# Optimization experiments

Hardware: AMD Instinct MI355X
Metric: run time of the kernel (lower is better)

Reference implementation:

```python
import jax, jax.numpy as jnp
import numpy as np

B, C, H, W = 2, 256, 128, 128
L, NH, NP = 4, 8, 4
D = C // NH
HW = H * W


def _pos_emb_2d(h, w, c):
    # positional_encodings.PositionalEncoding2D for channels-last input (B, h, w, c)
    ch = int(np.ceil(c / 4) * 2)
    inv_freq = 1.0 / (10000.0 ** (np.arange(0, ch, 2, dtype=np.float32) / ch))

    def emb(n):
        s = np.arange(n, dtype=np.float32)[:, None] * inv_freq[None, :]
        return np.stack([np.sin(s), np.cos(s)], -1).reshape(n, -1)  # interleaved sin/cos

    out = np.zeros((h, w, 2 * ch), np.float32)
    out[:, :, :ch] = emb(h)[:, None, :]
    out[:, :, ch:2 * ch] = emb(w)[None, :, :]
    return jnp.asarray(out[:, :, :c])


def _offset_bias():
    # init_weights grid_init bias of sampling_offsets
    thetas = np.arange(NH, dtype=np.float32) * (2.0 * np.pi / NH)
    g = np.stack([np.cos(thetas), np.sin(thetas)], -1)
    g = g / np.abs(g).max(-1, keepdims=True)
    g = np.tile(g[:, None, None, :], (1, 1, NP, 1))
    for i in range(NP):
        g[:, :, i, :] *= i + 1
    return np.tile(g.reshape(-1)[None], (L, 1)).astype(np.float32)


def _ref_points(h, w):
    # get_reference_points with scale_ratio == 1 (ratio of equal lidar ranges)
    ry, rx = jnp.meshgrid(jnp.linspace(0.5, h - 0.5, h) / h,
                          jnp.linspace(0.5, w - 0.5, w) / w, indexing='ij')
    return jnp.stack([rx.reshape(-1), ry.reshape(-1)], -1)  # (HW, 2) as (x, y)


def _deform_attn(value, loc, aw, h, w):
    # value: (B,HW,NH,D); loc in [0,1]: (B,HW,NH,NP,2); aw: (B,HW,NH,NP)
    # Matches F.grid_sample(mode='bilinear', padding_mode='zeros', align_corners=False)
    b, q, nh, d = value.shape
    p = loc.shape[3]
    v = value.transpose(0, 2, 1, 3)  # (B, NH, HW, D)
    gx = 2.0 * loc[..., 0] - 1.0
    gy = 2.0 * loc[..., 1] - 1.0
    ix = ((gx + 1.0) * w - 1.0) * 0.5
    iy = ((gy + 1.0) * h - 1.0) * 0.5
    x0 = jnp.floor(ix)
    y0 = jnp.floor(iy)

    def gather(xf, yf):
        valid = (xf >= 0) & (xf <= w - 1) & (yf >= 0) & (yf <= h - 1)
        xi = jnp.clip(xf, 0, w - 1).astype(jnp.int32)
        yi = jnp.clip(yf, 0, h - 1).astype(jnp.int32)
        idx = (yi * w + xi).transpose(0, 2, 1, 3).reshape(b, nh, q * p)
        g = jnp.take_along_axis(v, idx[..., None], axis=2).reshape(b, nh, q, p, d)
        return g * valid.transpose(0, 2, 1, 3)[..., None]

    wx1 = (ix - x0).transpose(0, 2, 1, 3)[..., None]
    wy1 = (iy - y0).transpose(0, 2, 1, 3)[..., None]
    wx0 = 1.0 - wx1
    wy0 = 1.0 - wy1
    s = (gather(x0, y0) * (wx0 * wy0) + gather(x0 + 1.0, y0) * (wx1 * wy0)
         + gather(x0, y0 + 1.0) * (wx0 * wy1) + gather(x0 + 1.0, y0 + 1.0) * (wx1 * wy1))
    out = jnp.einsum('bhqpd,bqhp->bqhd', s, aw)
    return out.reshape(b, q, nh * d)


def setup_inputs() -> dict:
    key = jax.random.key(0)
    ks = jax.random.split(key, 8)
    sc = 1.0 / np.sqrt(C).astype(np.float32)
    return {
        "ego_feature": jax.random.normal(ks[0], (B, C, H, W), jnp.float32),
        "conv_w": jax.random.normal(ks[1], (C, C), jnp.float32) * sc,  # 1x1 conv, (in,out)
        "conv_b": jnp.zeros((C,), jnp.float32),
        "in_scale": jnp.ones((1,), jnp.float32) / 30.0,
        "out_scale": jnp.ones((1,), jnp.float32) / 30.0,
        "off_w": jax.random.normal(ks[2], (L, C, NH * NP * 2), jnp.float32) * 0.01,
        "off_b": jnp.asarray(_offset_bias()),
        "aw_w": jax.random.normal(ks[3], (L, C, NH * NP), jnp.float32) * 0.02,
        "aw_b": jnp.zeros((L, NH * NP), jnp.float32),
        "vp_w": jax.random.normal(ks[4], (L, C, C), jnp.float32) * sc,
        "vp_b": jnp.zeros((L, C), jnp.float32),
        "op_w": jax.random.normal(ks[5], (L, C, C), jnp.float32) * sc,
        "op_b": jnp.zeros((L, C), jnp.float32),
    }


def reference(ego_feature, conv_w, conv_b, in_scale, out_scale, off_w, off_b,
              aw_w, aw_b, vp_w, vp_b, op_w, op_b):
    # PositionalEncodingPermute2D: channels-last PE, permuted to (C,H,W)
    pe_in = _pos_emb_2d(H, W, C).transpose(2, 0, 1)[None]  # (1,C,H,W)
    x = ego_feature + in_scale[0] * pe_in
    key_tok = x.reshape(B, C, HW).transpose(0, 2, 1)  # (B, HW, C)
    # Upsample(scale=1) is identity; 1x1 conv == per-token matmul
    out = key_tok @ conv_w + conv_b
    pe_out = _pos_emb_2d(H, W, C)[None]  # (1,H,W,C)
    ref = _ref_points(H, W)
    norm = jnp.asarray([W, H], jnp.float32)
    for l in range(L):
        o = out.reshape(B, H, W, C) + out_scale[0] * pe_out
        q = o.reshape(B, HW, C)
        identity = q
        v = (key_tok @ vp_w[l] + vp_b[l]).reshape(B, HW, NH, D)
        offs = (q @ off_w[l] + off_b[l]).reshape(B, HW, NH, NP, 2)
        aw = jax.nn.softmax((q @ aw_w[l] + aw_b[l]).reshape(B, HW, NH, NP), axis=-1)
        loc = ref[None, :, None, None, :] + offs / norm
        attn = _deform_attn(v, loc, aw, H, W)
        out = attn @ op_w[l] + op_b[l] + identity  # dropout is identity in eval
    return out  # (B, HW, C)
```

## Files before the change

kernel.cpp:

```cpp
#include <hip/hip_runtime.h>
#include <math.h>

#define HH 128
#define WW 128
#define CCH 256
#define NHH 8
#define NPP 4
#define DDIM 32
#define HWW (HH * WW)
#define BB 2
#define MM (BB * HWW)
#define KK 256

typedef __attribute__((ext_vector_type(8))) __bf16 bf16x8;
typedef __attribute__((ext_vector_type(8))) short s16x8;
typedef __attribute__((ext_vector_type(4))) short s16x4;
typedef __attribute__((ext_vector_type(4))) float f32x4;

#define PE_LOG2_STEP 0.20762050593f

__device__ __forceinline__ float pe_val(int c, int y, int x) {
    int j = (c & 127) >> 1;
    float pos = (c < 128) ? (float)y : (float)x;
    float f = exp2f(-(float)j * PE_LOG2_STEP);
    float s, cs;
    __sincosf(pos * f, &s, &cs);
    return (c & 1) ? cs : s;
}

__device__ __forceinline__ short f2b(float f) {
    union { float f; unsigned u; } c; c.f = f;
    unsigned r = c.u + 0x7FFF + ((c.u >> 16) & 1);
    return (short)(r >> 16);
}

__device__ __forceinline__ float b2f(short s) {
    union { unsigned u; float f; } c;
    c.u = ((unsigned)(unsigned short)s) << 16;
    return c.f;
}

__device__ __forceinline__ void gload16(const short* g, short* l) {
    __builtin_amdgcn_global_load_lds(
        (const __attribute__((address_space(1))) unsigned int*)g,
        (__attribute__((address_space(3))) unsigned int*)l, 16, 0, 0);
}

__global__ __launch_bounds__(256) void pe_table_kernel(
    const float* __restrict__ out_scale, short* __restrict__ pe_b)
{
    int t = blockIdx.x * 256 + threadIdx.x;
    int cp = t & 127;
    int p = t >> 7;
    int y = p >> 7, x = p & 127;
    int c2 = cp * 2;
    int j = (c2 & 127) >> 1;
    float pos = (c2 < 128) ? (float)y : (float)x;
    float f = exp2f(-(float)j * PE_LOG2_STEP);
    float s, c;
    __sincosf(pos * f, &s, &c);
    float sc = out_scale[0];
    pe_b[(size_t)p * CCH + c2] = f2b(sc * s);
    pe_b[(size_t)p * CCH + c2 + 1] = f2b(sc * c);
}

__global__ __launch_bounds__(256) void convert_big_w(
    const float* __restrict__ conv_w, const float* __restrict__ vp_w,
    const float* __restrict__ op_w, short* __restrict__ wt)
{
    __shared__ float tile[32][33];
    int z = blockIdx.z;
    const float* src = (z == 0) ? conv_w
                     : (z <= 4) ? vp_w + (size_t)(z - 1) * KK * CCH
                                : op_w + (size_t)(z - 5) * KK * CCH;
    short* dst = wt + (size_t)z * KK * CCH;
    int k0 = blockIdx.x * 32, n0 = blockIdx.y * 32;
    int tx = threadIdx.x, ty = threadIdx.y;
    #pragma unroll
    for (int i = 0; i < 4; ++i)
        tile[ty + i * 8][tx] = src[(size_t)(k0 + ty + i * 8) * CCH + n0 + tx];
    __syncthreads();
    int t = ty * 32 + tx;
    int n_l = t >> 3, ks = (t & 7) * 4;
    s16x4 o;
    #pragma unroll
    for (int j = 0; j < 4; ++j) o[j] = f2b(tile[ks + j][n_l]);
    *(s16x4*)&dst[(size_t)(n0 + n_l) * KK + k0 + ks] = o;
}

__global__ __launch_bounds__(256) void convert_offaw_w(
    const float* __restrict__ off_w, const float* __restrict__ aw_w,
    const float* __restrict__ off_b, const float* __restrict__ aw_b,
    short* __restrict__ wt, float* __restrict__ bias_cat)
{
    __shared__ float tile[32][33];
    int l = blockIdx.z;
    int nt = blockIdx.y;
    int k0 = blockIdx.x * 32;
    const float* src; int N, ncol0;
    if (nt < 2) { src = off_w + (size_t)l * KK * 64; N = 64; ncol0 = nt * 32; }
    else        { src = aw_w + (size_t)l * KK * 32; N = 32; ncol0 = 0; }
    int tx = threadIdx.x, ty = threadIdx.y;
    #pragma unroll
    for (int i = 0; i < 4; ++i)
        tile[ty + i * 8][tx] = src[(size_t)(k0 + ty + i * 8) * N + ncol0 + tx];
    __syncthreads();
    int t = ty * 32 + tx;
    int n_l = t >> 3, ks = (t & 7) * 4;
    s16x4 o;
    #pragma unroll
    for (int j = 0; j < 4; ++j) o[j] = f2b(tile[ks + j][n_l]);
    *(s16x4*)&wt[((size_t)l * 96 + nt * 32 + n_l) * KK + k0 + ks] = o;
    if (blockIdx.x == 0 && t < 32) {
        int col = nt * 32 + t;
        bias_cat[l * 96 + col] = (nt < 2) ? off_b[l * 64 + ncol0 + t]
                                          : aw_b[l * 32 + t];
    }
}

__global__ __launch_bounds__(256) void transpose_pe_kernel(
    const float* __restrict__ ego, const float* __restrict__ in_scale,
    short* __restrict__ ktb)
{
    __shared__ float tile[32][33];
    int b = blockIdx.z;
    int c0 = blockIdx.x * 32;
    int p0 = blockIdx.y * 32;
    int tx = threadIdx.x, ty = threadIdx.y;
    const float* egob = ego + (size_t)b * CCH * HWW;
    #pragma unroll
    for (int i = 0; i < 4; ++i)
        tile[ty + i * 8][tx] = egob[(size_t)(c0 + ty + i * 8) * HWW + p0 + tx];
    __syncthreads();
    float isc = in_scale[0];
    int t = ty * 32 + tx;
    int p_l = t >> 3, cs = (t & 7) * 4;
    int p = p0 + p_l;
    int y = p >> 7, x = p & 127;
    s16x4 o;
    #pragma unroll
    for (int j = 0; j < 4; ++j) {
        int c = c0 + cs + j;
        o[j] = f2b(tile[cs + j][p_l] + isc * pe_val(c, y, x));
    }
    *(s16x4*)&ktb[((size_t)b * HWW + p) * CCH + c0 + cs] = o;
}

__device__ __forceinline__ void stage_slab64(
    const short* __restrict__ src, short* As, int m0, int w, int lane)
{
    #pragma unroll
    for (int i = 0; i < 8; ++i) {
        int c = w * 64 + i * 256;
        int cc = c + lane;
        int r = cc >> 5, col = cc & 31, ks = col >> 3, u = col & 7;
        gload16(src + (size_t)(m0 + r) * KK + ks * 64 + ((u ^ (r & 7)) << 3),
                As + c * 8);
    }
}

template<int NINST>
__device__ __forceinline__ void stage_tile(
    const short* __restrict__ src, short* dst, int row0, int ks, int w, int lane)
{
    #pragma unroll
    for (int i = 0; i < NINST; ++i) {
        int c = w * 64 + i * 256;
        int cc = c + lane;
        int r = cc >> 3, u = cc & 7;
        gload16(src + (size_t)(row0 + r) * KK + ks * 64 + ((u ^ (r & 7)) << 3),
                dst + c * 8);
    }
}

template<int BM, int BN, int WM, int WN>
__device__ __forceinline__ void gemm_core_db(
    const short* __restrict__ A, const short* __restrict__ Bt,
    short* AsBase, short* BsBase, int m0, int n0, int tid,
    f32x4 (&acc)[WM / 16][WN / 16])
{
    constexpr int MF = WM / 16, NF = WN / 16;
    constexpr int WAVES_N = BN / WN;
    constexpr int A_INST = (BM * 8) / 256;
    constexpr int B_INST = (BN * 8) / 256;
    int w = tid >> 6, lane = tid & 63;
    int g = lane >> 4, l16 = lane & 15;
    int wr = w / WAVES_N, wc = w % WAVES_N;
    short* As0 = AsBase; short* As1 = AsBase + BM * 64;
    short* Bs0 = BsBase; short* Bs1 = BsBase + BN * 64;

    stage_tile<A_INST>(A, As0, m0, 0, w, lane);
    stage_tile<B_INST>(Bt, Bs0, n0, 0, w, lane);
    asm volatile("s_waitcnt vmcnt(0)" ::: "memory");
    __syncthreads();

    #pragma unroll
    for (int ks = 0; ks < 4; ++ks) {
        short* Ac = (ks & 1) ? As1 : As0;
        short* Bc = (ks & 1) ? Bs1 : Bs0;
        short* An = (ks & 1) ? As0 : As1;
        short* Bn = (ks & 1) ? Bs0 : Bs1;
        if (ks < 3) {
            stage_tile<A_INST>(A, An, m0, ks + 1, w, lane);
            stage_tile<B_INST>(Bt, Bn, n0, ks + 1, w, lane);
        }
        #pragma unroll
        for (int kh = 0; kh < 2; ++kh) {
            bf16x8 af[MF], bfr[NF];
            #pragma unroll
            for (int mf = 0; mf < MF; ++mf) {
                int r = wr * WM + mf * 16 + l16, s = kh * 4 + g;
                af[mf] = *(const bf16x8*)(Ac + r * 64 + ((s ^ (r & 7)) * 8));
            }
            #pragma unroll
            for (int nf = 0; nf < NF; ++nf) {
                int r = wc * WN + nf * 16 + l16, s = kh * 4 + g;
                bfr[nf] = *(const bf16x8*)(Bc + r * 64 + ((s ^ (r & 7)) * 8));
            }
            #pragma unroll
            for (int mf = 0; mf < MF; ++mf)
                #pragma unroll
                for (int nf = 0; nf < NF; ++nf)
                    acc[mf][nf] = __builtin_amdgcn_mfma_f32_16x16x32_bf16(
                        af[mf], bfr[nf], acc[mf][nf], 0, 0, 0);
        }
        if (ks < 3) {
            __builtin_amdgcn_sched_barrier(0);
            asm volatile("s_waitcnt vmcnt(0)" ::: "memory");
            __syncthreads();
        }
    }
}

__global__ __launch_bounds__(256) void gemm_conv_v(
    const short* __restrict__ ktb, const short* __restrict__ wt_big,
    const float* __restrict__ conv_b, const float* __restrict__ vp_b,
    const short* __restrict__ pe_b, short* __restrict__ qb,
    short* __restrict__ vb16)
{
    __shared__ short As[64 * 256];
    __shared__ short Bs[128 * 64];
    int tid = threadIdx.x;
    int w = tid >> 6, lane = tid & 63;
    int g = lane >> 4, l16 = lane & 15;
    int wr = w >> 1, wc = w & 1;
    int flat = blockIdx.x;
    int xcd = flat & 7;
    int idx = flat >> 3;
    int mloc = idx & 63;
    int n0 = (idx >> 6) * 128;
    int m0 = (xcd * 64 + mloc) * 64;

    stage_slab64(ktb, As, m0, w, lane);
    s16x8 rb[4];
    #pragma unroll
    for (int i = 0; i < 4; ++i) {
        int task = tid + i * 256; int r = task >> 3, s = task & 7;
        rb[i] = *(const s16x8*)(wt_big + (size_t)(n0 + r) * KK + s * 8);
    }
    asm volatile("s_waitcnt vmcnt(0)" ::: "memory");
    __syncthreads();

    bf16x8 afr[4][2][2];
    #pragma unroll
    for (int ks = 0; ks < 4; ++ks)
        #pragma unroll
        for (int kh = 0; kh < 2; ++kh)
            #pragma unroll
            for (int mf = 0; mf < 2; ++mf) {
                int s = kh * 4 + g;
                int r = wr * 32 + mf * 16 + l16;
                afr[ks][kh][mf] =
                    *(const bf16x8*)(As + r * 256 + (ks * 8 + (s ^ (r & 7))) * 8);
            }

    for (int z = 0; z < 5; ++z) {
        f32x4 acc[2][4] = {};
        #pragma unroll
        for (int ks = 0; ks < 4; ++ks) {
            __syncthreads();
            #pragma unroll
            for (int i = 0; i < 4; ++i) {
                int task = tid + i * 256; int r = task >> 3, s = task & 7;
                *(s16x8*)&Bs[r * 64 + ((s ^ (r & 7)) * 8)] = rb[i];
            }
            __syncthreads();
            if (ks < 3) {
                const short* Bz = wt_big + (size_t)z * KK * CCH;
                #pragma unroll
                for (int i = 0; i < 4; ++i) {
                    int task = tid + i * 256; int r = task >> 3, s = task & 7;
                    rb[i] = *(const s16x8*)(Bz + (size_t)(n0 + r) * KK + (ks + 1) * 64 + s * 8);
                }
            } else if (z < 4) {
                const short* Bz = wt_big + (size_t)(z + 1) * KK * CCH;
                #pragma unroll
                for (int i = 0; i < 4; ++i) {
                    int task = tid + i * 256; int r = task >> 3, s = task & 7;
                    rb[i] = *(const s16x8*)(Bz + (size_t)(n0 + r) * KK + s * 8);
                }
            }
            #pragma unroll
            for (int kh = 0; kh < 2; ++kh) {
                int s = kh * 4 + g;
                bf16x8 bfr[4];
                #pragma unroll
                for (int nf = 0; nf < 4; ++nf) {
                    int r = wc * 64 + nf * 16 + l16;
                    bfr[nf] = *(const bf16x8*)(Bs + r * 64 + ((s ^ (r & 7)) * 8));
                }
                #pragma unroll
                for (int mf = 0; mf < 2; ++mf)
                    #pragma unroll
                    for (int nf = 0; nf < 4; ++nf)
                        acc[mf][nf] = __builtin_amdgcn_mfma_f32_16x16x32_bf16(
                            afr[ks][kh][mf], bfr[nf], acc[mf][nf], 0, 0, 0);
            }
        }
        const float* bias = (z == 0) ? conv_b : vp_b + (size_t)(z - 1) * CCH;
        short* vz = vb16 + (size_t)(z - 1) * MM * CCH;
        #pragma unroll
        for (int mf = 0; mf < 2; ++mf) {
            #pragma unroll
            for (int nf = 0; nf < 4; ++nf) {
                int col = n0 + wc * 64 + nf * 16 + l16;
                float bv = bias[col];
                #pragma unroll
                for (int j = 0; j < 4; ++j) {
                    int row = m0 + wr * 32 + mf * 16 + g * 4 + j;
                    float vv = acc[mf][nf][j] + bv;
                    if (z == 0) {
                        int p = row & (HWW - 1);
                        qb[(size_t)row * CCH + col] =
                            f2b(vv + b2f(pe_b[(size_t)p * CCH + col]));
                    } else {
                        int b = row >> 14, p = row & (HWW - 1);
                        int h = col >> 5, d = col & 31;
                        vz[(((size_t)(b * NHH + h)) * HWW + p) * DDIM + d] = f2b(vv);
                    }
                }
            }
        }
    }
}

__global__ __launch_bounds__(256) void gemm_scores(
    const short* __restrict__ qb, const short* __restrict__ wt,
    const float* __restrict__ bias, float* __restrict__ scores)
{
    __shared__ short As[2 * 64 * 64];
    __shared__ short Bs[2 * 96 * 64];
    int tid = threadIdx.x;
    int m0 = blockIdx.y * 64;
    f32x4 acc[2][3] = {};
    gemm_core_db<64, 96, 32, 48>(qb, wt, As, Bs, m0, 0, tid, acc);

    int w = tid >> 6, lane = tid & 63;
    int g = lane >> 4, l16 = lane & 15;
    int wr = w >> 1, wc = w & 1;
    #pragma unroll
    for (int mf = 0; mf < 2; ++mf) {
        #pragma unroll
        for (int nf = 0; nf < 3; ++nf) {
            int col = wc * 48 + nf * 16 + l16;
            float bv = bias[col];
            #pragma unroll
            for (int j = 0; j < 4; ++j) {
                int row = m0 + wr * 32 + mf * 16 + g * 4 + j;
                scores[(size_t)row * 96 + col] = acc[mf][nf][j] + bv;
            }
        }
    }
}

template<bool FINAL>
__global__ __launch_bounds__(256) void gemm_op(
    const short* __restrict__ attnb, const short* __restrict__ wt,
    const float* __restrict__ bias, const short* __restrict__ pe_b,
    float* __restrict__ outf, short* __restrict__ qb)
{
    __shared__ short As[2 * 128 * 64];
    __shared__ short Bs[2 * 128 * 64];
    int tid = threadIdx.x;
    int flat = blockIdx.x;
    int xcd = flat & 7;
    int idx = flat >> 3;
    int mloc = idx & 31;
    int n0 = (idx >> 5) * 128;
    int m0 = (xcd * 32 + mloc) * 128;
    f32x4 acc[4][4] = {};
    gemm_core_db<128, 128, 64, 64>(attnb, wt, As, Bs, m0, n0, tid, acc);

    int w = tid >> 6, lane = tid & 63;
    int g = lane >> 4, l16 = lane & 15;
    int wr = w >> 1, wc = w & 1;
    #pragma unroll
    for (int mf = 0; mf < 4; ++mf) {
        #pragma unroll
        for (int nf = 0; nf < 4; ++nf) {
            int col = n0 + wc * 64 + nf * 16 + l16;
            float bv = bias[col];
            #pragma unroll
            for (int j = 0; j < 4; ++j) {
                int row = m0 + wr * 64 + mf * 16 + g * 4 + j;
                float vv = acc[mf][nf][j] + bv + b2f(qb[(size_t)row * CCH + col]);
                if (FINAL) {
                    outf[(size_t)row * CCH + col] = vv;
                } else {
                    int p = row & (HWW - 1);
                    qb[(size_t)row * CCH + col] =
                        f2b(vv + b2f(pe_b[(size_t)p * CCH + col]));
                }
            }
        }
    }
}

__device__ __forceinline__ void fma8(uint4 u, float w, float* a) {
    a[0] = fmaf(__uint_as_float(u.x << 16), w, a[0]);
    a[1] = fmaf(__uint_as_float(u.x & 0xffff0000u), w, a[1]);
    a[2] = fmaf(__uint_as_float(u.y << 16), w, a[2]);
    a[3] = fmaf(__uint_as_float(u.y & 0xffff0000u), w, a[3]);
    a[4] = fmaf(__uint_as_float(u.z << 16), w, a[4]);
    a[5] = fmaf(__uint_as_float(u.z & 0xffff0000u), w, a[5]);
    a[6] = fmaf(__uint_as_float(u.w << 16), w, a[6]);
    a[7] = fmaf(__uint_as_float(u.w & 0xffff0000u), w, a[7]);
}

__global__ __launch_bounds__(256) void deform_kernel(
    const short* __restrict__ vb16, const float* __restrict__ scores,
    short* __restrict__ attnb)
{
    int tid = threadIdx.x;
    int gi = tid >> 2;
    int dl = (tid & 3) * 8;
    long gid = (long)blockIdx.x * 64 + gi;
    int h = (int)(gid & 7);
    long bp = gid >> 3;
    int p = (int)(bp & (HWW - 1));
    int b = (int)(bp >> 14);
    int y = p >> 7, x = p & 127;
    const float* srow = scores + bp * 96;
    float4 sc4 = *(const float4*)(srow + 64 + h * 4);
    float mx = fmaxf(fmaxf(sc4.x, sc4.y), fmaxf(sc4.z, sc4.w));
    float e0 = __expf(sc4.x - mx), e1 = __expf(sc4.y - mx);
    float e2 = __expf(sc4.z - mx), e3 = __expf(sc4.w - mx);
    float inv = 1.f / (e0 + e1 + e2 + e3);
    float wa4[4] = {e0 * inv, e1 * inv, e2 * inv, e3 * inv};
    float4 o01 = *(const float4*)(srow + h * 8);
    float4 o23 = *(const float4*)(srow + h * 8 + 4);
    float oxs[4] = {o01.x, o01.z, o23.x, o23.z};
    float oys[4] = {o01.y, o01.w, o23.y, o23.w};
    const short* vbase = vb16 + ((size_t)(b * NHH + h) * HWW) * DDIM + dl;
    float a[8] = {};
    #pragma unroll
    for (int pt = 0; pt < NPP; ++pt) {
        float wa = wa4[pt];
        float ix = (float)x + oxs[pt];
        float iy = (float)y + oys[pt];
        float x0f = floorf(ix), y0f = floorf(iy);
        float fx = ix - x0f, fy = iy - y0f;
        float wx0 = (x0f >= 0.f && x0f <= 127.f) ? (1.f - fx) : 0.f;
        float wx1 = (x0f >= -1.f && x0f <= 126.f) ? fx : 0.f;
        float wy0 = ((y0f >= 0.f && y0f <= 127.f) ? (1.f - fy) : 0.f) * wa;
        float wy1 = ((y0f >= -1.f && y0f <= 126.f) ? fy : 0.f) * wa;
        int xi0 = (int)fminf(fmaxf(x0f, 0.f), 127.f);
        int yi0 = (int)fminf(fmaxf(y0f, 0.f), 127.f);
        int xi1 = (int)fminf(fmaxf(x0f + 1.f, 0.f), 127.f);
        int yi1 = (int)fminf(fmaxf(y0f + 1.f, 0.f), 127.f);
        int r0 = yi0 << 7, r1 = yi1 << 7;
        uint4 u00 = *(const uint4*)(vbase + (size_t)(r0 + xi0) * DDIM);
        uint4 u01 = *(const uint4*)(vbase + (size_t)(r0 + xi1) * DDIM);
        uint4 u10 = *(const uint4*)(vbase + (size_t)(r1 + xi0) * DDIM);
        uint4 u11 = *(const uint4*)(vbase + (size_t)(r1 + xi1) * DDIM);
        fma8(u00, wx0 * wy0, a);
        fma8(u01, wx1 * wy0, a);
        fma8(u10, wx0 * wy1, a);
        fma8(u11, wx1 * wy1, a);
    }
    s16x8 o;
    #pragma unroll
    for (int j = 0; j < 8; ++j) o[j] = f2b(a[j]);
    *(s16x8*)&attnb[bp * CCH + h * DDIM + dl] = o;
}

extern "C" void kernel_launch(void* const* d_in, const int* in_sizes, int n_in,
                              void* d_out, int out_size, void* d_ws, size_t ws_size,
                              hipStream_t stream) {
    const float* ego       = (const float*)d_in[0];
    const float* conv_w    = (const float*)d_in[1];
    const float* conv_b    = (const float*)d_in[2];
    const float* in_scale  = (const float*)d_in[3];
    const float* out_scale = (const float*)d_in[4];
    const float* off_w     = (const float*)d_in[5];
    const float* off_b     = (const float*)d_in[6];
    const float* aw_w      = (const float*)d_in[7];
    const float* aw_b      = (const float*)d_in[8];
    const float* vp_w      = (const float*)d_in[9];
    const float* vp_b      = (const float*)d_in[10];
    const float* op_w      = (const float*)d_in[11];
    const float* op_b      = (const float*)d_in[12];
    float* out = (float*)d_out;

    float* scores   = (float*)d_ws;
    float* bias_cat = scores + (size_t)MM * 96;
    short* pe_b     = (short*)(bias_cat + 4 * 96);
    short* ktb      = pe_b + (size_t)HWW * CCH;
    short* qb       = ktb + (size_t)MM * CCH;
    short* vb16     = qb + (size_t)MM * CCH;
    short* attnb    = vb16 + (size_t)4 * MM * CCH;
    short* wt_big   = attnb + (size_t)MM * CCH;
    short* wt_offaw = wt_big + (size_t)9 * KK * CCH;

    pe_table_kernel<<<HWW * 128 / 256, 256, 0, stream>>>(out_scale, pe_b);
    convert_big_w<<<dim3(8, 8, 9), dim3(32, 8), 0, stream>>>(conv_w, vp_w, op_w, wt_big);
    convert_offaw_w<<<dim3(8, 3, 4), dim3(32, 8), 0, stream>>>(
        off_w, aw_w, off_b, aw_b, wt_offaw, bias_cat);
    transpose_pe_kernel<<<dim3(8, 512, 2), dim3(32, 8), 0, stream>>>(ego, in_scale, ktb);

    gemm_conv_v<<<1024, 256, 0, stream>>>(
        ktb, wt_big, conv_b, vp_b, pe_b, qb, vb16);

    for (int l = 0; l < 4; ++l) {
        gemm_scores<<<dim3(1, 512), 256, 0, stream>>>(
            qb, wt_offaw + (size_t)l * 96 * KK, bias_cat + l * 96, scores);
        deform_kernel<<<MM * NHH / 64, 256, 0, stream>>>(
            vb16 + (size_t)l * MM * CCH, scores, attnb);
        if (l < 3) {
            gemm_op<false><<<512, 256, 0, stream>>>(
                attnb, wt_big + (size_t)(5 + l) * KK * CCH, op_b + l * CCH,
                pe_b, nullptr, qb);
        } else {
            gemm_op<true><<<512, 256, 0, stream>>>(
                attnb, wt_big + (size_t)(5 + l) * KK * CCH, op_b + l * CCH,
                pe_b, out, qb);
        }
    }
}
```

Measured before the change: 213.7 us.

## Fuse offset/weight score GEMM into deformable sampling kernel via shared memory

Merges the per-layer score GEMM (offsets and attention logits) with the deformable bilinear sampling kernel, so scores stay in shared memory instead of round-tripping through a global buffer. Each block now computes 64 query rows of scores, then each thread loops over all 8 heads serially. This removes one launch and the score write/read per layer. In exchange, parallelism drops from 4096 blocks to 512, each thread does 8x more gather work in sequence, and the GEMM and gather phases no longer overlap across blocks, so there is less latency hiding for the random value gathers.

```diff
diff --git a/kernel.cpp b/kernel.cpp
--- a/kernel.cpp
+++ b/kernel.cpp
@@ -344,35 +344,6 @@
     }
 }
 
-__global__ __launch_bounds__(256) void gemm_scores(
-    const short* __restrict__ qb, const short* __restrict__ wt,
-    const float* __restrict__ bias, float* __restrict__ scores)
-{
-    __shared__ short As[2 * 64 * 64];
-    __shared__ short Bs[2 * 96 * 64];
-    int tid = threadIdx.x;
-    int m0 = blockIdx.y * 64;
-    f32x4 acc[2][3] = {};
-    gemm_core_db<64, 96, 32, 48>(qb, wt, As, Bs, m0, 0, tid, acc);
-
-    int w = tid >> 6, lane = tid & 63;
-    int g = lane >> 4, l16 = lane & 15;
-    int wr = w >> 1, wc = w & 1;
-    #pragma unroll
-    for (int mf = 0; mf < 2; ++mf) {
-        #pragma unroll
-        for (int nf = 0; nf < 3; ++nf) {
-            int col = wc * 48 + nf * 16 + l16;
-            float bv = bias[col];
-            #pragma unroll
-            for (int j = 0; j < 4; ++j) {
-                int row = m0 + wr * 32 + mf * 16 + g * 4 + j;
-                scores[(size_t)row * 96 + col] = acc[mf][nf][j] + bv;
-            }
-        }
-    }
-}
-
 template<bool FINAL>
 __global__ __launch_bounds__(256) void gemm_op(
     const short* __restrict__ attnb, const short* __restrict__ wt,
@@ -427,61 +398,88 @@
     a[7] = fmaf(__uint_as_float(u.w & 0xffff0000u), w, a[7]);
 }
 
-__global__ __launch_bounds__(256) void deform_kernel(
-    const short* __restrict__ vb16, const float* __restrict__ scores,
+__global__ __launch_bounds__(256) void scores_deform(
+    const short* __restrict__ qb, const short* __restrict__ wt,
+    const float* __restrict__ bias, const short* __restrict__ vb16,
     short* __restrict__ attnb)
 {
+    __shared__ short smem[2 * 64 * 64 + 2 * 96 * 64];
+    short* As = smem;
+    short* Bs = smem + 2 * 64 * 64;
     int tid = threadIdx.x;
-    int gi = tid >> 2;
+    int m0 = blockIdx.x * 64;
+    f32x4 acc[2][3] = {};
+    gemm_core_db<64, 96, 32, 48>(qb, wt, As, Bs, m0, 0, tid, acc);
+
+    int w = tid >> 6, lane = tid & 63;
+    int g = lane >> 4, l16 = lane & 15;
+    int wr = w >> 1, wc = w & 1;
+    __syncthreads();
+    float* sc = (float*)smem;
+    #pragma unroll
+    for (int mf = 0; mf < 2; ++mf) {
+        #pragma unroll
+        for (int nf = 0; nf < 3; ++nf) {
+            int col = wc * 48 + nf * 16 + l16;
+            float bv = bias[col];
+            #pragma unroll
+            for (int j = 0; j < 4; ++j) {
+                int rl = wr * 32 + mf * 16 + g * 4 + j;
+                sc[rl * 100 + col] = acc[mf][nf][j] + bv;
+            }
+        }
+    }
+    __syncthreads();
+
+    int r = tid >> 2;
     int dl = (tid & 3) * 8;
-    long gid = (long)blockIdx.x * 64 + gi;
-    int h = (int)(gid & 7);
-    long bp = gid >> 3;
-    int p = (int)(bp & (HWW - 1));
-    int b = (int)(bp >> 14);
+    int row = m0 + r;
+    int b = row >> 14, p = row & (HWW - 1);
     int y = p >> 7, x = p & 127;
-    const float* srow = scores + bp * 96;
-    float4 sc4 = *(const float4*)(srow + 64 + h * 4);
-    float mx = fmaxf(fmaxf(sc4.x, sc4.y), fmaxf(sc4.z, sc4.w));
-    float e0 = __expf(sc4.x - mx), e1 = __expf(sc4.y - mx);
-    float e2 = __expf(sc4.z - mx), e3 = __expf(sc4.w - mx);
-    float inv = 1.f / (e0 + e1 + e2 + e3);
-    float wa4[4] = {e0 * inv, e1 * inv, e2 * inv, e3 * inv};
-    float4 o01 = *(const float4*)(srow + h * 8);
-    float4 o23 = *(const float4*)(srow + h * 8 + 4);
-    float oxs[4] = {o01.x, o01.z, o23.x, o23.z};
-    float oys[4] = {o01.y, o01.w, o23.y, o23.w};
-    const short* vbase = vb16 + ((size_t)(b * NHH + h) * HWW) * DDIM + dl;
-    float a[8] = {};
-    #pragma unroll
-    for (int pt = 0; pt < NPP; ++pt) {
-        float wa = wa4[pt];
-        float ix = (float)x + oxs[pt];
-        float iy = (float)y + oys[pt];
-        float x0f = floorf(ix), y0f = floorf(iy);
-        float fx = ix - x0f, fy = iy - y0f;
-        float wx0 = (x0f >= 0.f && x0f <= 127.f) ? (1.f - fx) : 0.f;
-        float wx1 = (x0f >= -1.f && x0f <= 126.f) ? fx : 0.f;
-        float wy0 = ((y0f >= 0.f && y0f <= 127.f) ? (1.f - fy) : 0.f) * wa;
-        float wy1 = ((y0f >= -1.f && y0f <= 126.f) ? fy : 0.f) * wa;
-        int xi0 = (int)fminf(fmaxf(x0f, 0.f), 127.f);
-        int yi0 = (int)fminf(fmaxf(y0f, 0.f), 127.f);
-        int xi1 = (int)fminf(fmaxf(x0f + 1.f, 0.f), 127.f);
-        int yi1 = (int)fminf(fmaxf(y0f + 1.f, 0.f), 127.f);
-        int r0 = yi0 << 7, r1 = yi1 << 7;
-        uint4 u00 = *(const uint4*)(vbase + (size_t)(r0 + xi0) * DDIM);
-        uint4 u01 = *(const uint4*)(vbase + (size_t)(r0 + xi1) * DDIM);
-        uint4 u10 = *(const uint4*)(vbase + (size_t)(r1 + xi0) * DDIM);
-        uint4 u11 = *(const uint4*)(vbase + (size_t)(r1 + xi1) * DDIM);
-        fma8(u00, wx0 * wy0, a);
-        fma8(u01, wx1 * wy0, a);
-        fma8(u10, wx0 * wy1, a);
-        fma8(u11, wx1 * wy1, a);
-    }
-    s16x8 o;
-    #pragma unroll
-    for (int j = 0; j < 8; ++j) o[j] = f2b(a[j]);
-    *(s16x8*)&attnb[bp * CCH + h * DDIM + dl] = o;
+    const float* srow = sc + r * 100;
+    for (int h = 0; h < NHH; ++h) {
+        float4 sc4 = *(const float4*)(srow + 64 + h * 4);
+        float mx = fmaxf(fmaxf(sc4.x, sc4.y), fmaxf(sc4.z, sc4.w));
+        float e0 = __expf(sc4.x - mx), e1 = __expf(sc4.y - mx);
+        float e2 = __expf(sc4.z - mx), e3 = __expf(sc4.w - mx);
+        float inv = 1.f / (e0 + e1 + e2 + e3);
+        float wa4[4] = {e0 * inv, e1 * inv, e2 * inv, e3 * inv};
+        float4 o01 = *(const float4*)(srow + h * 8);
+        float4 o23 = *(const float4*)(srow + h * 8 + 4);
+        float oxs[4] = {o01.x, o01.z, o23.x, o23.z};
+        float oys[4] = {o01.y, o01.w, o23.y, o23.w};
+        const short* vbase = vb16 + ((size_t)(b * NHH + h) * HWW) * DDIM + dl;
+        float a[8] = {};
+        #pragma unroll
+        for (int pt = 0; pt < NPP; ++pt) {
+            float wa = wa4[pt];
+            float ix = (float)x + oxs[pt];
+            float iy = (float)y + oys[pt];
+            float x0f = floorf(ix), y0f = floorf(iy);
+            float fx = ix - x0f, fy = iy - y0f;
+            float wx0 = (x0f >= 0.f && x0f <= 127.f) ? (1.f - fx) : 0.f;
+            float wx1 = (x0f >= -1.f && x0f <= 126.f) ? fx : 0.f;
+            float wy0 = ((y0f >= 0.f && y0f <= 127.f) ? (1.f - fy) : 0.f) * wa;
+            float wy1 = ((y0f >= -1.f && y0f <= 126.f) ? fy : 0.f) * wa;
+            int xi0 = (int)fminf(fmaxf(x0f, 0.f), 127.f);
+            int yi0 = (int)fminf(fmaxf(y0f, 0.f), 127.f);
+            int xi1 = (int)fminf(fmaxf(x0f + 1.f, 0.f), 127.f);
+            int yi1 = (int)fminf(fmaxf(y0f + 1.f, 0.f), 127.f);
+            int r0 = yi0 << 7, r1 = yi1 << 7;
+            uint4 u00 = *(const uint4*)(vbase + (size_t)(r0 + xi0) * DDIM);
+            uint4 u01 = *(const uint4*)(vbase + (size_t)(r0 + xi1) * DDIM);
+            uint4 u10 = *(const uint4*)(vbase + (size_t)(r1 + xi0) * DDIM);
+            uint4 u11 = *(const uint4*)(vbase + (size_t)(r1 + xi1) * DDIM);
+            fma8(u00, wx0 * wy0, a);
+            fma8(u01, wx1 * wy0, a);
+            fma8(u10, wx0 * wy1, a);
+            fma8(u11, wx1 * wy1, a);
+        }
+        s16x8 o;
+        #pragma unroll
+        for (int j = 0; j < 8; ++j) o[j] = f2b(a[j]);
+        *(s16x8*)&attnb[(size_t)row * CCH + h * DDIM + dl] = o;
+    }
 }
 
 extern "C" void kernel_launch(void* const* d_in, const int* in_sizes, int n_in,
@@ -502,8 +500,7 @@
     const float* op_b      = (const float*)d_in[12];
     float* out = (float*)d_out;
 
-    float* scores   = (float*)d_ws;
-    float* bias_cat = scores + (size_t)MM * 96;
+    float* bias_cat = (float*)d_ws;
     short* pe_b     = (short*)(bias_cat + 4 * 96);
     short* ktb      = pe_b + (size_t)HWW * CCH;
     short* qb       = ktb + (size_t)MM * CCH;
@@ -522,10 +519,9 @@
         ktb, wt_big, conv_b, vp_b, pe_b, qb, vb16);
 
     for (int l = 0; l < 4; ++l) {
-        gemm_scores<<<dim3(1, 512), 256, 0, stream>>>(
-            qb, wt_offaw + (size_t)l * 96 * KK, bias_cat + l * 96, scores);
-        deform_kernel<<<MM * NHH / 64, 256, 0, stream>>>(
-            vb16 + (size_t)l * MM * CCH, scores, attnb);
+        scores_deform<<<MM / 64, 256, 0, stream>>>(
+            qb, wt_offaw + (size_t)l * 96 * KK, bias_cat + l * 96,
+            vb16 + (size_t)l * MM * CCH, attnb);
         if (l < 3) {
             gemm_op<false><<<512, 256, 0, stream>>>(
                 attnb, wt_big + (size_t)(5 + l) * KK * CCH, op_b + l * CCH,
```

New measurement: 217.1 us. About the same (+1.6%).
